# Optimization experiments

Hardware: AMD Instinct MI355X
Metric: run time of the kernel (lower is better)

## Reference

```python
import jax, jax.numpy as jnp
import numpy as np

N_API, N_FILE, E = 50000, 20000, 250000
N_INP, N_OUT, H = 512, 256, 3


def setup_inputs() -> dict:
    key = jax.random.key(0)
    ks = jax.random.split(key, 16)
    s = 0.05
    return {
        "emb_api": jax.random.normal(ks[0], (N_API, N_INP), jnp.float32),
        "emb_file": jax.random.normal(ks[1], (N_FILE, N_INP), jnp.float32),
        "e_tensor": jax.random.normal(ks[2], (E,), jnp.float32),
        "src": jax.random.randint(ks[3], (E,), 0, N_API, jnp.int32),
        "dst": jax.random.randint(ks[4], (E,), 0, N_FILE, jnp.int32),
        # api_proj / file_proj (Linear n_inp->n_inp), stored as [in,out]
        "Wapi": jax.random.normal(ks[5], (N_INP, N_INP), jnp.float32) * s,
        "bapi": jnp.zeros((N_INP,), jnp.float32),
        "Wfile": jax.random.normal(ks[6], (N_INP, N_INP), jnp.float32) * s,
        "bfile": jnp.zeros((N_INP,), jnp.float32),
        # GATConv fc_src / fc_dst (no bias), attn vectors, output bias
        "Wsrc": jax.random.normal(ks[7], (N_INP, H * N_OUT), jnp.float32) * s,
        "Wdst": jax.random.normal(ks[8], (N_INP, H * N_OUT), jnp.float32) * s,
        "attn_l": jax.random.normal(ks[9], (H, N_OUT), jnp.float32) * s,
        "attn_r": jax.random.normal(ks[10], (H, N_OUT), jnp.float32) * s,
        "gat_bias": jnp.zeros((H * N_OUT,), jnp.float32),
        # head_linear (3*n_out -> n_out)
        "Whead": jax.random.normal(ks[11], (H * N_OUT, N_OUT), jnp.float32) * s,
        "bhead": jnp.zeros((N_OUT,), jnp.float32),
    }


def reference(emb_api, emb_file, e_tensor, src, dst,
              Wapi, bapi, Wfile, bfile,
              Wsrc, Wdst, attn_l, attn_r, gat_bias,
              Whead, bhead):
    nd = emb_file.shape[0]
    # dual linear projections
    x_api = emb_api @ Wapi + bapi            # [Nsrc, n_inp]
    x_file = emb_file @ Wfile + bfile        # [Ndst, n_inp]
    # GATConv (bipartite, DGL semantics): per-head linear, additive attention
    fsrc = (x_api @ Wsrc).reshape(-1, H, N_OUT)   # [Nsrc, H, D]
    fdst = (x_file @ Wdst).reshape(-1, H, N_OUT)  # [Ndst, H, D]
    el = jnp.sum(fsrc * attn_l, axis=-1)          # [Nsrc, H]
    er = jnp.sum(fdst * attn_r, axis=-1)          # [Ndst, H]
    e = jax.nn.leaky_relu(el[src] + er[dst], 0.2)  # [E, H]
    # edge softmax over incoming edges of each dst node
    m = jax.ops.segment_max(e, dst, num_segments=nd)   # [Ndst, H]
    a = jnp.exp(e - m[dst])
    z = jax.ops.segment_sum(a, dst, num_segments=nd)   # [Ndst, H]
    alpha = a / z[dst]                                  # [E, H]
    # weighted aggregation of source messages
    rst = jax.ops.segment_sum(alpha[:, :, None] * fsrc[src], dst,
                              num_segments=nd)          # [Ndst, H, D]
    rst = rst + gat_bias.reshape(H, N_OUT)
    # head fusion
    z_str = rst.reshape(nd, H * N_OUT) @ Whead + bhead  # [Ndst, n_out]
    return z_str
```

## Files before the change

kernel.cpp:

```cpp
#include <hip/hip_runtime.h>
#include <hip/hip_bf16.h>
#include <cstdint>
#include <cstddef>

#define N_INP 512
#define N_OUT 256
#define H 3
#define HD (H * N_OUT)
#define AGG_D (H * (N_INP + 1))
#define HSTR 522
#define KP 1568

typedef __attribute__((ext_vector_type(8))) short short8;
typedef __attribute__((ext_vector_type(4))) float f32x4;

__device__ inline unsigned short f2bf(float x) {
    union { float f; unsigned u; } v; v.f = x;
    unsigned r = v.u + 0x7fffu + ((v.u >> 16) & 1u);
    return (unsigned short)(r >> 16);
}
__device__ inline float bflo2f(unsigned u) {
    union { unsigned u; float f; } v; v.u = u << 16; return v.f;
}
__device__ inline float bfhi2f(unsigned u) {
    union { unsigned u; float f; } v; v.u = u & 0xffff0000u; return v.f;
}

__global__ void zero_int_kernel(int* p, int n) {
    int i = blockIdx.x * blockDim.x + threadIdx.x;
    if (i < n) p[i] = 0;
}

__global__ __launch_bounds__(256) void v_kernel(
    const float* __restrict__ Wsrc, const float* __restrict__ Wdst,
    const float* __restrict__ attn_l, const float* __restrict__ attn_r,
    float* __restrict__ v) {
    int wave = threadIdx.x >> 6, lane = threadIdx.x & 63;
    int idx = blockIdx.x * 4 + wave;
    if (idx >= 2 * H * N_INP) return;
    int which = idx / (H * N_INP);
    int r = idx % (H * N_INP);
    int h = r / N_INP, o = r % N_INP;
    const float* W = which ? Wdst : Wsrc;
    const float* at = which ? attn_r : attn_l;
    float s = 0.f;
#pragma unroll
    for (int i = 0; i < N_OUT / 64; ++i) {
        int t = lane + i * 64;
        s += W[(size_t)o * HD + h * N_OUT + t] * at[h * N_OUT + t];
    }
#pragma unroll
    for (int off = 32; off >= 1; off >>= 1) s += __shfl_xor(s, off, 64);
    if (lane == 0) v[idx] = s;
}

__global__ __launch_bounds__(256) void u_kernel(
    const float* __restrict__ Wapi, const float* __restrict__ Wfile,
    const float* __restrict__ bapi, const float* __restrict__ bfile,
    const float* __restrict__ v, float* __restrict__ u,
    float* __restrict__ ebias) {
    int wave = threadIdx.x >> 6, lane = threadIdx.x & 63;
    int idx = blockIdx.x * 4 + wave;
    if (idx < 2 * H * N_INP) {
        int which = idx / (H * N_INP);
        int r = idx % (H * N_INP);
        int h = r / N_INP, i = r % N_INP;
        const float* W = which ? Wfile : Wapi;
        const float* vv = v + which * (H * N_INP) + h * N_INP;
        float s = 0.f;
#pragma unroll
        for (int j = 0; j < N_INP / 64; ++j) {
            int o = lane + j * 64;
            s += W[(size_t)i * N_INP + o] * vv[o];
        }
#pragma unroll
        for (int off = 32; off >= 1; off >>= 1) s += __shfl_xor(s, off, 64);
        if (lane == 0) u[idx] = s;
    } else if (idx < 2 * H * N_INP + 6) {
        int k = idx - 2 * H * N_INP;
        int which = k / H, h = k % H;
        const float* b = which ? bfile : bapi;
        const float* vv = v + which * (H * N_INP) + h * N_INP;
        float s = 0.f;
#pragma unroll
        for (int j = 0; j < N_INP / 64; ++j) {
            int o = lane + j * 64;
            s += b[o] * vv[o];
        }
#pragma unroll
        for (int off = 32; off >= 1; off >>= 1) s += __shfl_xor(s, off, 64);
        if (lane == 0) ebias[k] = s;
    }
}

__global__ __launch_bounds__(256) void elr_kernel(
    const float* __restrict__ emb, const float* __restrict__ u,
    const float* __restrict__ ebias, float* __restrict__ out,
    unsigned short* __restrict__ embB, int n) {
    __shared__ float su[H * N_INP];
    for (int i = threadIdx.x; i < H * N_INP; i += 256) su[i] = u[i];
    __syncthreads();
    int wave = threadIdx.x >> 6;
    int lane = threadIdx.x & 63;
    int node = blockIdx.x * 4 + wave;
    if (node >= n) return;
    const float4* row = (const float4*)(emb + (size_t)node * N_INP);
    float4 v0 = row[lane];
    float4 v1 = row[64 + lane];
    int c0 = lane * 4, c1 = 256 + lane * 4;
    if (embB) {
        unsigned short* o = embB + (size_t)node * N_INP;
        ushort4 p0, p1;
        p0.x = f2bf(v0.x); p0.y = f2bf(v0.y); p0.z = f2bf(v0.z); p0.w = f2bf(v0.w);
        p1.x = f2bf(v1.x); p1.y = f2bf(v1.y); p1.z = f2bf(v1.z); p1.w = f2bf(v1.w);
        *(ushort4*)(o + c0) = p0;
        *(ushort4*)(o + c1) = p1;
    }
    float d[H];
#pragma unroll
    for (int h = 0; h < H; ++h) {
        const float* uh = su + h * N_INP;
        d[h] = v0.x * uh[c0] + v0.y * uh[c0 + 1] + v0.z * uh[c0 + 2] + v0.w * uh[c0 + 3]
             + v1.x * uh[c1] + v1.y * uh[c1 + 1] + v1.z * uh[c1 + 2] + v1.w * uh[c1 + 3];
#pragma unroll
        for (int off = 32; off >= 1; off >>= 1) d[h] += __shfl_xor(d[h], off, 64);
    }
    if (lane == 0) {
#pragma unroll
        for (int h = 0; h < H; ++h) out[(size_t)node * H + h] = d[h] + ebias[h];
    }
}

__global__ void count_kernel(const int* __restrict__ dst, int* __restrict__ counts, int E) {
    int e = blockIdx.x * blockDim.x + threadIdx.x;
    if (e < E) atomicAdd(&counts[dst[e]], 1);
}

__global__ __launch_bounds__(1024) void scan_kernel(const int* __restrict__ counts,
                                                    int* __restrict__ offsets,
                                                    int* __restrict__ cursor, int n) {
    __shared__ int part[1024];
    int t = threadIdx.x;
    const int CH = (n + 1023) / 1024;
    int lo = t * CH, hi = min(lo + CH, n);
    int s = 0;
    for (int i = lo; i < hi; ++i) s += counts[i];
    part[t] = s;
    __syncthreads();
    for (int off = 1; off < 1024; off <<= 1) {
        int v = (t >= off) ? part[t - off] : 0;
        __syncthreads();
        part[t] += v;
        __syncthreads();
    }
    int base = (t == 0) ? 0 : part[t - 1];
    for (int i = lo; i < hi; ++i) {
        offsets[i] = base; cursor[i] = base;
        base += counts[i];
    }
    if (t == 1023) offsets[n] = part[1023];
}

__global__ void scatter_kernel(const int* __restrict__ src, const int* __restrict__ dst,
                               int* __restrict__ cursor, int* __restrict__ csr_src, int E) {
    int e = blockIdx.x * blockDim.x + threadIdx.x;
    if (e < E) {
        int slot = atomicAdd(&cursor[dst[e]], 1);
        csr_src[slot] = src[e];
    }
}

__global__ __launch_bounds__(256) void alpha_kernel(
    const int* __restrict__ offsets, const int* __restrict__ csr_src,
    const float* __restrict__ el, const float* __restrict__ er,
    float* __restrict__ alpha, int nd) {
    int wave = threadIdx.x >> 6;
    int lane = threadIdx.x & 63;
    int d = blockIdx.x * 4 + wave;
    if (d >= nd) return;
    int lo = offsets[d], hi = offsets[d + 1];
    if (lo == hi) return;
    float er0 = er[(size_t)d * H + 0], er1 = er[(size_t)d * H + 1], er2 = er[(size_t)d * H + 2];
    float m0 = -3.4e38f, m1 = -3.4e38f, m2 = -3.4e38f;
    for (int s = lo + lane; s < hi; s += 64) {
        int u = csr_src[s];
        float e0 = el[(size_t)u * H + 0] + er0; e0 = e0 >= 0.f ? e0 : 0.2f * e0;
        float e1 = el[(size_t)u * H + 1] + er1; e1 = e1 >= 0.f ? e1 : 0.2f * e1;
        float e2 = el[(size_t)u * H + 2] + er2; e2 = e2 >= 0.f ? e2 : 0.2f * e2;
        m0 = fmaxf(m0, e0); m1 = fmaxf(m1, e1); m2 = fmaxf(m2, e2);
    }
#pragma unroll
    for (int off = 32; off >= 1; off >>= 1) {
        m0 = fmaxf(m0, __shfl_xor(m0, off, 64));
        m1 = fmaxf(m1, __shfl_xor(m1, off, 64));
        m2 = fmaxf(m2, __shfl_xor(m2, off, 64));
    }
    float s0 = 0.f, s1 = 0.f, s2 = 0.f;
    for (int s = lo + lane; s < hi; s += 64) {
        int u = csr_src[s];
        float e0 = el[(size_t)u * H + 0] + er0; e0 = e0 >= 0.f ? e0 : 0.2f * e0;
        float e1 = el[(size_t)u * H + 1] + er1; e1 = e1 >= 0.f ? e1 : 0.2f * e1;
        float e2 = el[(size_t)u * H + 2] + er2; e2 = e2 >= 0.f ? e2 : 0.2f * e2;
        float a0 = expf(e0 - m0), a1 = expf(e1 - m1), a2 = expf(e2 - m2);
        alpha[(size_t)s * H + 0] = a0; alpha[(size_t)s * H + 1] = a1; alpha[(size_t)s * H + 2] = a2;
        s0 += a0; s1 += a1; s2 += a2;
    }
#pragma unroll
    for (int off = 32; off >= 1; off >>= 1) {
        s0 += __shfl_xor(s0, off, 64);
        s1 += __shfl_xor(s1, off, 64);
        s2 += __shfl_xor(s2, off, 64);
    }
    float i0 = 1.f / s0, i1 = 1.f / s1, i2 = 1.f / s2;
    for (int s = lo + lane; s < hi; s += 64) {
        alpha[(size_t)s * H + 0] *= i0;
        alpha[(size_t)s * H + 1] *= i1;
        alpha[(size_t)s * H + 2] *= i2;
    }
}

__global__ __launch_bounds__(256) void agg_kernel(
    const int* __restrict__ offsets, const int* __restrict__ csr_src,
    const float* __restrict__ alpha, const unsigned short* __restrict__ embB,
    unsigned short* __restrict__ aggB, int nd) {
    int d = blockIdx.x;
    if (d >= nd) return;
    int tid = threadIdx.x;
    int lo = offsets[d], hi = offsets[d + 1];
    int c = tid * 2;
    float a00 = 0.f, a01 = 0.f, a10 = 0.f, a11 = 0.f, a20 = 0.f, a21 = 0.f;
    for (int s = lo; s < hi; ++s) {
        int u = csr_src[s];
        float w0 = alpha[(size_t)s * H + 0];
        float w1 = alpha[(size_t)s * H + 1];
        float w2 = alpha[(size_t)s * H + 2];
        unsigned v = *(const unsigned*)(embB + (size_t)u * N_INP + c);
        float x = bflo2f(v), y = bfhi2f(v);
        a00 += w0 * x; a01 += w0 * y;
        a10 += w1 * x; a11 += w1 * y;
        a20 += w2 * x; a21 += w2 * y;
    }
    size_t base = (size_t)d * KP;
    *(unsigned*)(aggB + base + 0 * HSTR + c) = (unsigned)f2bf(a00) | ((unsigned)f2bf(a01) << 16);
    *(unsigned*)(aggB + base + 1 * HSTR + c) = (unsigned)f2bf(a10) | ((unsigned)f2bf(a11) << 16);
    *(unsigned*)(aggB + base + 2 * HSTR + c) = (unsigned)f2bf(a20) | ((unsigned)f2bf(a21) << 16);
    if (tid == 0) {
        unsigned short flag = (hi > lo) ? (unsigned short)0x3f80 : (unsigned short)0;
#pragma unroll
        for (int h = 0; h < H; ++h) {
            aggB[base + h * HSTR + 512] = flag;
            for (int z = 513; z < HSTR; ++z) aggB[base + h * HSTR + z] = 0;
        }
        aggB[base + 3 * HSTR + 0] = 0;
        aggB[base + 3 * HSTR + 1] = 0;
    }
}

template <int K>
__global__ __launch_bounds__(256) void wgemm(
    const float* __restrict__ A, int lda, size_t sAz,
    const float* __restrict__ B, int ldb, size_t sBz,
    float* __restrict__ C, int ldc, size_t sCz, int M) {
    A += blockIdx.z * sAz; B += blockIdx.z * sBz; C += blockIdx.z * sCz;
    __shared__ float sA[8 * K];
    __shared__ float red[8 * 256];
    int tid = threadIdx.x;
    int r0 = blockIdx.x * 8;
    int bn = blockIdx.y * 64;
    for (int i = tid; i < 8 * K; i += 256) {
        int r = i / K, k = i % K;
        sA[i] = A[(size_t)(r0 + r) * lda + k];
    }
    __syncthreads();
    int cl = tid & 63, ks = tid >> 6;
    int col = bn + cl;
    const int KC = K / 4;
    float acc[8] = {};
    for (int k0 = ks * KC; k0 < ks * KC + KC; k0 += 8) {
        float b[8];
#pragma unroll
        for (int j = 0; j < 8; ++j) b[j] = B[(size_t)(k0 + j) * ldb + col];
#pragma unroll
        for (int j = 0; j < 8; ++j) {
            float bb = b[j];
#pragma unroll
            for (int i = 0; i < 8; ++i) acc[i] += sA[i * K + k0 + j] * bb;
        }
    }
#pragma unroll
    for (int i = 0; i < 8; ++i) red[i * 256 + ks * 64 + cl] = acc[i];
    __syncthreads();
    for (int t = tid; t < 512; t += 256) {
        int i = t >> 6, c = t & 63;
        float s = red[i * 256 + c] + red[i * 256 + 64 + c]
                + red[i * 256 + 128 + c] + red[i * 256 + 192 + c];
        if (r0 + i < M) C[(size_t)(r0 + i) * ldc + bn + c] = s;
    }
}

__global__ __launch_bounds__(256) void brow_kernel(
    const float* __restrict__ bapi, const float* __restrict__ T,
    const float* __restrict__ gat_bias, const float* __restrict__ Whead,
    const float* __restrict__ bhead,
    float* __restrict__ Mmat, float* __restrict__ bz) {
    int wave = threadIdx.x >> 6, lane = threadIdx.x & 63;
    int idx = blockIdx.x * 4 + wave;
    if (idx < H * N_OUT) {
        int h = idx / N_OUT, j = idx % N_OUT;
        float s = 0.f;
#pragma unroll
        for (int i = 0; i < N_INP / 64; ++i) {
            int cc = lane + i * 64;
            s += bapi[cc] * T[((size_t)h * N_INP + cc) * N_OUT + j];
        }
#pragma unroll
        for (int off = 32; off >= 1; off >>= 1) s += __shfl_xor(s, off, 64);
        if (lane == 0) Mmat[((size_t)(h * 513 + 512)) * N_OUT + j] = s;
    } else if (idx < H * N_OUT + N_OUT) {
        int j = idx - H * N_OUT;
        float s = 0.f;
#pragma unroll
        for (int i = 0; i < HD / 64; ++i) {
            int f = lane + i * 64;
            s += gat_bias[f] * Whead[(size_t)f * N_OUT + j];
        }
#pragma unroll
        for (int off = 32; off >= 1; off >>= 1) s += __shfl_xor(s, off, 64);
        if (lane == 0) bz[j] = s + bhead[j];
    }
}

__global__ void convT_kernel(const float* __restrict__ Mmat, unsigned short* __restrict__ MmatT) {
    int idx = blockIdx.x * blockDim.x + threadIdx.x;
    if (idx >= N_OUT * KP) return;
    int n = idx / KP, k = idx % KP;
    float v = 0.f;
    if (k < H * HSTR) {
        int h = k / HSTR, c = k % HSTR;
        if (c < 513) v = Mmat[((size_t)(h * 513 + c)) * N_OUT + n];
    }
    MmatT[(size_t)n * KP + k] = f2bf(v);
}

__global__ __launch_bounds__(256) void gemm_mfma(
    const unsigned short* __restrict__ A, const unsigned short* __restrict__ BT,
    const float* __restrict__ bias, float* __restrict__ C, int M) {
    __shared__ short As[128 * 40];
    __shared__ short Bs[128 * 40];
    int tid = threadIdx.x;
    int wave = tid >> 6, lane = tid & 63;
    int bm = blockIdx.y * 128, bn = blockIdx.x * 128;
    int wm = (wave >> 1) * 64, wn = (wave & 1) * 64;
    int quad = lane >> 4, m16 = lane & 15;
    f32x4 acc[4][4] = {};
    int r0 = tid >> 2;
    int cg = tid & 3;
    for (int k0 = 0; k0 < KP; k0 += 32) {
#pragma unroll
        for (int p = 0; p < 2; ++p) {
            int row = r0 + p * 64;
            int gr = bm + row;
            short8 av = {};
            if (gr < M) av = *(const short8*)(A + (size_t)gr * KP + k0 + cg * 8);
            *(short8*)(&As[row * 40 + cg * 8]) = av;
            short8 bv = *(const short8*)(BT + (size_t)(bn + row) * KP + k0 + cg * 8);
            *(short8*)(&Bs[row * 40 + cg * 8]) = bv;
        }
        __syncthreads();
        short8 af[4], bf[4];
#pragma unroll
        for (int t = 0; t < 4; ++t) {
            af[t] = *(const short8*)(&As[(wm + t * 16 + m16) * 40 + quad * 8]);
            bf[t] = *(const short8*)(&Bs[(wn + t * 16 + m16) * 40 + quad * 8]);
        }
#pragma unroll
        for (int mt = 0; mt < 4; ++mt)
#pragma unroll
            for (int nt = 0; nt < 4; ++nt)
                acc[mt][nt] = __builtin_amdgcn_mfma_f32_16x16x32_bf16(
                    af[mt], bf[nt], acc[mt][nt], 0, 0, 0);
        __syncthreads();
    }
#pragma unroll
    for (int mt = 0; mt < 4; ++mt) {
#pragma unroll
        for (int i = 0; i < 4; ++i) {
            int r = bm + wm + mt * 16 + quad * 4 + i;
            if (r >= M) continue;
#pragma unroll
            for (int nt = 0; nt < 4; ++nt) {
                int col = bn + wn + nt * 16 + m16;
                C[(size_t)r * N_OUT + col] = acc[mt][nt][i] + bias[col];
            }
        }
    }
}

extern "C" void kernel_launch(void* const* d_in, const int* in_sizes, int n_in,
                              void* d_out, int out_size, void* d_ws, size_t ws_size,
                              hipStream_t stream) {
    const float* emb_api  = (const float*)d_in[0];
    const float* emb_file = (const float*)d_in[1];
    const int*   src      = (const int*)d_in[3];
    const int*   dst      = (const int*)d_in[4];
    const float* Wapi     = (const float*)d_in[5];
    const float* bapi     = (const float*)d_in[6];
    const float* Wfile    = (const float*)d_in[7];
    const float* bfile    = (const float*)d_in[8];
    const float* Wsrc     = (const float*)d_in[9];
    const float* Wdst     = (const float*)d_in[10];
    const float* attn_l   = (const float*)d_in[11];
    const float* attn_r   = (const float*)d_in[12];
    const float* gat_bias = (const float*)d_in[13];
    const float* Whead    = (const float*)d_in[14];
    const float* bhead    = (const float*)d_in[15];
    float* out = (float*)d_out;

    const int NAPI = in_sizes[0] / N_INP;
    const int NFIL = in_sizes[1] / N_INP;
    const int E    = in_sizes[3];

    char* p = (char*)d_ws;
    auto alloc = [&](size_t bytes) -> void* {
        void* r = (void*)p;
        p += (bytes + 255) & ~(size_t)255;
        return r;
    };
    float* el      = (float*)alloc((size_t)NAPI * H * 4);
    float* er      = (float*)alloc((size_t)NFIL * H * 4);
    float* vbuf    = (float*)alloc(2 * H * N_INP * 4);
    float* ubuf    = (float*)alloc(2 * H * N_INP * 4);
    float* ebias   = (float*)alloc(8 * 4);
    float* T       = (float*)alloc((size_t)H * N_INP * N_OUT * 4);
    float* Mmat    = (float*)alloc((size_t)AGG_D * N_OUT * 4);
    float* bz      = (float*)alloc(N_OUT * 4);
    int*   counts  = (int*)alloc((size_t)NFIL * 4);
    int*   offsets = (int*)alloc((size_t)(NFIL + 1) * 4);
    int*   cursor  = (int*)alloc((size_t)NFIL * 4);
    int*   csr_src = (int*)alloc((size_t)E * 4);
    float* alphaB  = (float*)alloc((size_t)E * H * 4);
    unsigned short* embB  = (unsigned short*)alloc((size_t)NAPI * N_INP * 2);
    unsigned short* aggB  = (unsigned short*)alloc((size_t)NFIL * KP * 2);
    unsigned short* MmatT = (unsigned short*)alloc((size_t)N_OUT * KP * 2);
    (void)ws_size; (void)n_in; (void)out_size;

    v_kernel<<<(2 * H * N_INP + 3) / 4, 256, 0, stream>>>(Wsrc, Wdst, attn_l, attn_r, vbuf);
    u_kernel<<<(2 * H * N_INP + 6 + 3) / 4, 256, 0, stream>>>(Wapi, Wfile, bapi, bfile, vbuf, ubuf, ebias);
    wgemm<N_OUT><<<dim3(N_INP / 8, 4, H), 256, 0, stream>>>(
        Wsrc, HD, (size_t)N_OUT,
        Whead, N_OUT, (size_t)N_OUT * N_OUT,
        T, N_OUT, (size_t)N_INP * N_OUT, N_INP);
    wgemm<N_INP><<<dim3(N_INP / 8, 4, H), 256, 0, stream>>>(
        Wapi, N_INP, (size_t)0,
        T, N_OUT, (size_t)N_INP * N_OUT,
        Mmat, N_OUT, (size_t)513 * N_OUT, N_INP);
    brow_kernel<<<(H * N_OUT + N_OUT + 3) / 4, 256, 0, stream>>>(
        bapi, T, gat_bias, Whead, bhead, Mmat, bz);
    convT_kernel<<<(N_OUT * KP + 255) / 256, 256, 0, stream>>>(Mmat, MmatT);

    elr_kernel<<<(NAPI + 3) / 4, 256, 0, stream>>>(emb_api, ubuf, ebias, el, embB, NAPI);
    elr_kernel<<<(NFIL + 3) / 4, 256, 0, stream>>>(emb_file, ubuf + H * N_INP, ebias + 3, er, nullptr, NFIL);

    zero_int_kernel<<<(NFIL + 255) / 256, 256, 0, stream>>>(counts, NFIL);
    count_kernel<<<(E + 255) / 256, 256, 0, stream>>>(dst, counts, E);
    scan_kernel<<<1, 1024, 0, stream>>>(counts, offsets, cursor, NFIL);
    scatter_kernel<<<(E + 255) / 256, 256, 0, stream>>>(src, dst, cursor, csr_src, E);

    alpha_kernel<<<(NFIL + 3) / 4, 256, 0, stream>>>(offsets, csr_src, el, er, alphaB, NFIL);
    agg_kernel<<<NFIL, 256, 0, stream>>>(offsets, csr_src, alphaB, embB, aggB, NFIL);

    gemm_mfma<<<dim3(256 / 128, (NFIL + 127) / 128), 256, 0, stream>>>(
        aggB, MmatT, bz, out, NFIL);
}
```

Measured before the change: 485.3 us.

## Split-K final GEMM with async LDS double-buffering and atomic accumulation

After: 490.7 us. No clear change (+1.1%).

```diff
diff --git a/kernel.cpp b/kernel.cpp
--- a/kernel.cpp
+++ b/kernel.cpp
@@ -26,9 +26,20 @@
     union { unsigned u; float f; } v; v.u = u & 0xffff0000u; return v.f;
 }
 
+__device__ inline void glds16(const void* g, void* l) {
+    __builtin_amdgcn_global_load_lds(
+        (const __attribute__((address_space(1))) void*)g,
+        (__attribute__((address_space(3))) void*)l, 16, 0, 0);
+}
+
 __global__ void zero_int_kernel(int* p, int n) {
     int i = blockIdx.x * blockDim.x + threadIdx.x;
     if (i < n) p[i] = 0;
+}
+
+__global__ void initC_kernel(float* __restrict__ C, const float* __restrict__ bz, int n) {
+    int i = blockIdx.x * blockDim.x + threadIdx.x;
+    if (i < n) C[i] = bz[i & (N_OUT - 1)];
 }
 
 __global__ __launch_bounds__(256) void v_kernel(
@@ -342,36 +353,52 @@
     MmatT[(size_t)n * KP + k] = f2bf(v);
 }
 
-__global__ __launch_bounds__(256) void gemm_mfma(
+__global__ __launch_bounds__(256, 4) void gemm_mfma(
     const unsigned short* __restrict__ A, const unsigned short* __restrict__ BT,
-    const float* __restrict__ bias, float* __restrict__ C, int M) {
-    __shared__ short As[128 * 40];
-    __shared__ short Bs[128 * 40];
+    float* __restrict__ C, int M) {
+    __shared__ __align__(16) short As[2][128 * 32];
+    __shared__ __align__(16) short Bs[2][128 * 32];
     int tid = threadIdx.x;
     int wave = tid >> 6, lane = tid & 63;
     int bm = blockIdx.y * 128, bn = blockIdx.x * 128;
     int wm = (wave >> 1) * 64, wn = (wave & 1) * 64;
     int quad = lane >> 4, m16 = lane & 15;
+    int kz = blockIdx.z;
+    int kbeg = kz * 416;
+    int kend = (kz == 3) ? KP : kbeg + 416;
+
+    int srow = lane >> 2;
+    int schunk = (lane & 3) * 8;
+
     f32x4 acc[4][4] = {};
-    int r0 = tid >> 2;
-    int cg = tid & 3;
-    for (int k0 = 0; k0 < KP; k0 += 32) {
+
+    auto stage = [&](int buf, int k0) {
 #pragma unroll
         for (int p = 0; p < 2; ++p) {
-            int row = r0 + p * 64;
-            int gr = bm + row;
-            short8 av = {};
-            if (gr < M) av = *(const short8*)(A + (size_t)gr * KP + k0 + cg * 8);
-            *(short8*)(&As[row * 40 + cg * 8]) = av;
-            short8 bv = *(const short8*)(BT + (size_t)(bn + row) * KP + k0 + cg * 8);
-            *(short8*)(&Bs[row * 40 + cg * 8]) = bv;
-        }
-        __syncthreads();
+            int row = p * 64 + wave * 16 + srow;
+            int ar = bm + row; if (ar >= M) ar = M - 1;
+            glds16(A + (size_t)ar * KP + k0 + schunk, &As[buf][(p * 64 + wave * 16) * 32]);
+            glds16(BT + (size_t)(bn + row) * KP + k0 + schunk, &Bs[buf][(p * 64 + wave * 16) * 32]);
+        }
+    };
+
+    stage(0, kbeg);
+    int cur = 0;
+    for (int k0 = kbeg; k0 < kend; k0 += 32) {
+        if (k0 + 32 < kend) {
+            stage(cur ^ 1, k0 + 32);
+            asm volatile("s_waitcnt vmcnt(4)" ::: "memory");
+        } else {
+            asm volatile("s_waitcnt vmcnt(0)" ::: "memory");
+        }
+        asm volatile("" ::: "memory");
+        __builtin_amdgcn_s_barrier();
+        asm volatile("" ::: "memory");
         short8 af[4], bf[4];
 #pragma unroll
         for (int t = 0; t < 4; ++t) {
-            af[t] = *(const short8*)(&As[(wm + t * 16 + m16) * 40 + quad * 8]);
-            bf[t] = *(const short8*)(&Bs[(wn + t * 16 + m16) * 40 + quad * 8]);
+            af[t] = *(const short8*)(&As[cur][(wm + t * 16 + m16) * 32 + quad * 8]);
+            bf[t] = *(const short8*)(&Bs[cur][(wn + t * 16 + m16) * 32 + quad * 8]);
         }
 #pragma unroll
         for (int mt = 0; mt < 4; ++mt)
@@ -379,7 +406,10 @@
             for (int nt = 0; nt < 4; ++nt)
                 acc[mt][nt] = __builtin_amdgcn_mfma_f32_16x16x32_bf16(
                     af[mt], bf[nt], acc[mt][nt], 0, 0, 0);
-        __syncthreads();
+        asm volatile("" ::: "memory");
+        __builtin_amdgcn_s_barrier();
+        asm volatile("" ::: "memory");
+        cur ^= 1;
     }
 #pragma unroll
     for (int mt = 0; mt < 4; ++mt) {
@@ -390,7 +420,7 @@
 #pragma unroll
             for (int nt = 0; nt < 4; ++nt) {
                 int col = bn + wn + nt * 16 + m16;
-                C[(size_t)r * N_OUT + col] = acc[mt][nt][i] + bias[col];
+                atomicAdd(&C[(size_t)r * N_OUT + col], acc[mt][nt][i]);
             }
         }
     }
@@ -457,6 +487,7 @@
     brow_kernel<<<(H * N_OUT + N_OUT + 3) / 4, 256, 0, stream>>>(
         bapi, T, gat_bias, Whead, bhead, Mmat, bz);
     convT_kernel<<<(N_OUT * KP + 255) / 256, 256, 0, stream>>>(Mmat, MmatT);
+    initC_kernel<<<((size_t)NFIL * N_OUT + 255) / 256, 256, 0, stream>>>(out, bz, NFIL * N_OUT);
 
     elr_kernel<<<(NAPI + 3) / 4, 256, 0, stream>>>(emb_api, ubuf, ebias, el, embB, NAPI);
     elr_kernel<<<(NFIL + 3) / 4, 256, 0, stream>>>(emb_file, ubuf + H * N_INP, ebias + 3, er, nullptr, NFIL);
@@ -469,6 +500,6 @@
     alpha_kernel<<<(NFIL + 3) / 4, 256, 0, stream>>>(offsets, csr_src, el, er, alphaB, NFIL);
     agg_kernel<<<NFIL, 256, 0, stream>>>(offsets, csr_src, alphaB, embB, aggB, NFIL);
 
-    gemm_mfma<<<dim3(256 / 128, (NFIL + 127) / 128), 256, 0, stream>>>(
-        aggB, MmatT, bz, out, NFIL);
-}
+    gemm_mfma<<<dim3(256 / 128, (NFIL + 127) / 128, 4), 256, 0, stream>>>(
+        aggB, MmatT, out, NFIL);
+}
```

## Retile head GEMM to 32x256 blocks with double-buffered register prefetch

Applied to the files above, without the earlier changes.

Measured after the change: 462.1 us. 4.8% less time.

```diff
diff --git a/kernel.cpp b/kernel.cpp
--- a/kernel.cpp
+++ b/kernel.cpp
@@ -10,6 +10,7 @@
 #define AGG_D (H * (N_INP + 1))
 #define HSTR 522
 #define KP 1568
+#define GEMM_NT (KP / 32)
 
 typedef __attribute__((ext_vector_type(8))) short short8;
 typedef __attribute__((ext_vector_type(4))) float f32x4;
@@ -345,52 +346,95 @@
 __global__ __launch_bounds__(256) void gemm_mfma(
     const unsigned short* __restrict__ A, const unsigned short* __restrict__ BT,
     const float* __restrict__ bias, float* __restrict__ C, int M) {
-    __shared__ short As[128 * 40];
-    __shared__ short Bs[128 * 40];
+    __shared__ __align__(16) short As[2][32 * 32];
+    __shared__ __align__(16) short Bs[2][256 * 32];
     int tid = threadIdx.x;
     int wave = tid >> 6, lane = tid & 63;
-    int bm = blockIdx.y * 128, bn = blockIdx.x * 128;
-    int wm = (wave >> 1) * 64, wn = (wave & 1) * 64;
+    int bm = blockIdx.x * 32;
+    int wn = wave * 64;
     int quad = lane >> 4, m16 = lane & 15;
-    f32x4 acc[4][4] = {};
-    int r0 = tid >> 2;
-    int cg = tid & 3;
-    for (int k0 = 0; k0 < KP; k0 += 32) {
-#pragma unroll
-        for (int p = 0; p < 2; ++p) {
-            int row = r0 + p * 64;
-            int gr = bm + row;
-            short8 av = {};
-            if (gr < M) av = *(const short8*)(A + (size_t)gr * KP + k0 + cg * 8);
-            *(short8*)(&As[row * 40 + cg * 8]) = av;
-            short8 bv = *(const short8*)(BT + (size_t)(bn + row) * KP + k0 + cg * 8);
-            *(short8*)(&Bs[row * 40 + cg * 8]) = bv;
-        }
-        __syncthreads();
-        short8 af[4], bf[4];
-#pragma unroll
-        for (int t = 0; t < 4; ++t) {
-            af[t] = *(const short8*)(&As[(wm + t * 16 + m16) * 40 + quad * 8]);
-            bf[t] = *(const short8*)(&Bs[(wn + t * 16 + m16) * 40 + quad * 8]);
-        }
-#pragma unroll
-        for (int mt = 0; mt < 4; ++mt)
+
+    int srow = tid >> 2;
+    int schunk = (tid & 3) * 8;
+    bool doA = (tid < 128);
+    int arow_l = doA ? srow : 0;
+    int arow = bm + arow_l; if (arow >= M) arow = M - 1;
+    const unsigned short* Ap  = A + (size_t)arow * KP + schunk;
+    const unsigned short* Bp0 = BT + (size_t)(srow      ) * KP + schunk;
+    const unsigned short* Bp1 = BT + (size_t)(srow +  64) * KP + schunk;
+    const unsigned short* Bp2 = BT + (size_t)(srow + 128) * KP + schunk;
+    const unsigned short* Bp3 = BT + (size_t)(srow + 192) * KP + schunk;
+
+    f32x4 acc[2][4] = {};
+    short8 a0{}, b00{}, b01{}, b02{}, b03{};
+    short8 a1{}, b10{}, b11{}, b12{}, b13{};
+
+    auto LD = [&](short8& ra, short8& r0, short8& r1, short8& r2, short8& r3, int k0) {
+        if (doA) ra = *(const short8*)(Ap + k0);
+        r0 = *(const short8*)(Bp0 + k0);
+        r1 = *(const short8*)(Bp1 + k0);
+        r2 = *(const short8*)(Bp2 + k0);
+        r3 = *(const short8*)(Bp3 + k0);
+    };
+    auto WR = [&](int buf, short8 ra, short8 r0, short8 r1, short8 r2, short8 r3) {
+        if (doA) *(short8*)(&As[buf][arow_l * 32 + schunk]) = ra;
+        *(short8*)(&Bs[buf][(srow      ) * 32 + schunk]) = r0;
+        *(short8*)(&Bs[buf][(srow +  64) * 32 + schunk]) = r1;
+        *(short8*)(&Bs[buf][(srow + 128) * 32 + schunk]) = r2;
+        *(short8*)(&Bs[buf][(srow + 192) * 32 + schunk]) = r3;
+    };
+    auto FENCE = [&]() {
+        asm volatile("s_waitcnt lgkmcnt(0)" ::: "memory");
+        __builtin_amdgcn_sched_barrier(0);
+        __builtin_amdgcn_s_barrier();
+        __builtin_amdgcn_sched_barrier(0);
+    };
+
+    LD(a0, b00, b01, b02, b03, 0);
+    LD(a1, b10, b11, b12, b13, 32);
+    WR(0, a0, b00, b01, b02, b03);
+    LD(a0, b00, b01, b02, b03, 64);
+    FENCE();
+
+    for (int t = 0; t < GEMM_NT; ++t) {
+        int rb = t & 1;
+        short8 af[2], bf[4];
+#pragma unroll
+        for (int mt = 0; mt < 2; ++mt)
+            af[mt] = *(const short8*)(&As[rb][(mt * 16 + m16) * 32 + quad * 8]);
+#pragma unroll
+        for (int nt = 0; nt < 4; ++nt)
+            bf[nt] = *(const short8*)(&Bs[rb][(wn + nt * 16 + m16) * 32 + quad * 8]);
+        int k3 = (t + 3) * 32;
+        if (t & 1) {
+            if (t + 1 < GEMM_NT) WR(rb ^ 1, a0, b00, b01, b02, b03);
+            if (t + 3 < GEMM_NT) LD(a0, b00, b01, b02, b03, k3);
+        } else {
+            if (t + 1 < GEMM_NT) WR(rb ^ 1, a1, b10, b11, b12, b13);
+            if (t + 3 < GEMM_NT) LD(a1, b10, b11, b12, b13, k3);
+        }
+#pragma unroll
+        for (int mt = 0; mt < 2; ++mt)
 #pragma unroll
             for (int nt = 0; nt < 4; ++nt)
                 acc[mt][nt] = __builtin_amdgcn_mfma_f32_16x16x32_bf16(
                     af[mt], bf[nt], acc[mt][nt], 0, 0, 0);
-        __syncthreads();
-    }
-#pragma unroll
-    for (int mt = 0; mt < 4; ++mt) {
+        FENCE();
+    }
+
+    float bcol[4];
+#pragma unroll
+    for (int nt = 0; nt < 4; ++nt) bcol[nt] = bias[wn + nt * 16 + m16];
+#pragma unroll
+    for (int mt = 0; mt < 2; ++mt) {
 #pragma unroll
         for (int i = 0; i < 4; ++i) {
-            int r = bm + wm + mt * 16 + quad * 4 + i;
+            int r = bm + mt * 16 + quad * 4 + i;
             if (r >= M) continue;
 #pragma unroll
             for (int nt = 0; nt < 4; ++nt) {
-                int col = bn + wn + nt * 16 + m16;
-                C[(size_t)r * N_OUT + col] = acc[mt][nt][i] + bias[col];
+                int col = wn + nt * 16 + m16;
+                C[(size_t)r * N_OUT + col] = acc[mt][nt][i] + bcol[nt];
             }
         }
     }
@@ -469,6 +513,6 @@
     alpha_kernel<<<(NFIL + 3) / 4, 256, 0, stream>>>(offsets, csr_src, el, er, alphaB, NFIL);
     agg_kernel<<<NFIL, 256, 0, stream>>>(offsets, csr_src, alphaB, embB, aggB, NFIL);
 
-    gemm_mfma<<<dim3(256 / 128, (NFIL + 127) / 128), 256, 0, stream>>>(
+    gemm_mfma<<<dim3((NFIL + 31) / 32), 256, 0, stream>>>(
         aggB, MmatT, bz, out, NFIL);
 }
```
